# Kernel tuning notes

Measured on AMD Instinct MI355X. Metric: run time of the kernel, lower is better.

Reference implementation:

```python
import jax, jax.numpy as jnp
import numpy as np

B, CIN, H, W = 32, 64, 112, 112
COUT, KH, KW = 64, 3, 3
STRIDE = (1, 1)
PADDING = ((1, 1), (1, 1))
DILATION = (1, 1)


def setup_inputs() -> dict:
    key = jax.random.key(0)
    k1, k2, k3 = jax.random.split(key, 3)
    # quantized activations and weights, int8 value range [-128, 127]
    x_q = jax.random.randint(k1, (B, CIN, H, W), -128, 128, dtype=jnp.int32).astype(jnp.int8)
    w_q = jax.random.randint(k2, (COUT, CIN, KH, KW), -128, 128, dtype=jnp.int32).astype(jnp.int8)
    weight_scale = jnp.float32(0.02)   # per-tensor weight scale
    act_scale = jnp.float32(0.05)      # per-tensor activation scale
    bias = jax.random.normal(k3, (COUT,), dtype=jnp.float32)
    return {"x_q": x_q, "w_q": w_q, "weight_scale": weight_scale,
            "act_scale": act_scale, "bias": bias}


def reference(x_q, w_q, weight_scale, act_scale, bias):
    acc = jax.lax.conv_general_dilated(
        x_q.astype(jnp.int32), w_q.astype(jnp.int32),
        window_strides=STRIDE, padding=PADDING, rhs_dilation=DILATION,
        dimension_numbers=("NCHW", "OIHW", "NCHW"),
        preferred_element_type=jnp.int32)
    # fused dequant (per-tensor scales) + FP32 bias -> FP32 output [B, COUT, H, W]
    out = acc.astype(jnp.float32) * (act_scale * weight_scale) + bias[None, :, None, None]
    return out
```

## Files before the change

### kernel.cpp

```cpp
#include <hip/hip_runtime.h>
#include <stdint.h>

#define BATCH 32
#define CIN   64
#define HH    112
#define WW    112
#define COUT_ 64

typedef int v4i __attribute__((ext_vector_type(4)));

#define WT_OFF   0
#define ZP_OFF   36864
#define XT_OFF   65536
#define XT_NEED  (65536 + 26167296)

__global__ void wtrans_kernel(const int* __restrict__ wq, int8_t* __restrict__ wt) {
    int idx = blockIdx.x * 256 + threadIdx.x;
    int ci   = idx & 63;
    int khkw = (idx >> 6) % 9;
    int co   = idx / 576;
    wt[idx] = (int8_t)wq[co * 576 + ci * 9 + khkw];
}

__global__ void xtrans_kernel(const int* __restrict__ x, const int* __restrict__ wq,
                              int8_t* __restrict__ ws) {
    int8_t* __restrict__ xt = ws + XT_OFF;
    const int bid = blockIdx.x;
    const int tid = threadIdx.x;
    if (bid < 6272) {
        int idx  = bid * 256 + tid;
        int ci4  = idx & 15;
        int rest = idx >> 4;
        int cg   = rest % 28;
        int bh   = rest / 28;
        int h    = bh % 112;
        int b    = bh / 112;
        const v4i* gp = (const v4i*)(x + ((b * CIN + ci4 * 4) * HH + h) * WW + cg * 4);
        v4i q0 = gp[0];
        v4i q1 = gp[3136];
        v4i q2 = gp[2 * 3136];
        v4i q3 = gp[3 * 3136];
        int8_t* rowp = xt + (size_t)bh * 114 * 64;
        #pragma unroll
        for (int j = 0; j < 4; ++j) {
            uint32_t lo01 = __builtin_amdgcn_perm((uint32_t)q1[j], (uint32_t)q0[j], 0x0C0C0400u);
            uint32_t lo23 = __builtin_amdgcn_perm((uint32_t)q3[j], (uint32_t)q2[j], 0x04000C0Cu);
            int col = cg * 4 + 1 + j;
            int sd  = (((ci4 >> 2) ^ ((col >> 1) & 3)) << 2) | (ci4 & 3);
            *(uint32_t*)&rowp[col * 64 + sd * 4] = lo01 | lo23;
        }
    } else if (bid < 6720) {
        int idx  = (bid - 6272) * 256 + tid;
        int d    = idx & 15;
        int side = (idx >> 4) & 1;
        int bh   = idx >> 5;
        int col  = side ? 113 : 0;
        *(uint32_t*)&xt[((size_t)bh * 114 + col) * 64 + d * 4] = 0u;
    } else if (bid < 6728) {
        int idx = (bid - 6720) * 256 + tid;
        if (idx < 1824) *(uint32_t*)&ws[ZP_OFF + idx * 4] = 0u;
    } else {
        int idx  = (bid - 6728) * 256 + tid;
        int ci   = idx & 63;
        int khkw = (idx >> 6) % 9;
        int co   = idx / 576;
        ws[WT_OFF + idx] = (int8_t)wq[co * 576 + ci * 9 + khkw];
    }
}

__launch_bounds__(256, 4)
__global__ void conv2_kernel(const int8_t* __restrict__ ws,
                             const float*  __restrict__ wscale,
                             const float*  __restrict__ ascale,
                             const float*  __restrict__ bias,
                             float*        __restrict__ out) {
    __shared__ int8_t xs[4 * 114 * 64];

    const int tid = threadIdx.x;
    const int bt  = ((blockIdx.x & 7) * 224) + (blockIdx.x >> 3);
    const int b   = bt / 56;
    const int h0  = (bt % 56) * 2;

    const int8_t* __restrict__ xt = ws + XT_OFF;
    const int8_t* __restrict__ zp = ws + ZP_OFF;
    const int8_t* __restrict__ wt = ws + WT_OFF;

    const int lane = tid & 63;
    const int wave = tid >> 6;
    const int ln15 = lane & 15;
    const int quad = lane >> 4;

    const v4i* wrow = (const v4i*)(wt + (size_t)(wave * 16 + ln15) * 576);
    v4i a[9];
    #pragma unroll
    for (int t = 0; t < 9; ++t) a[t] = wrow[t * 4 + quad];

    #pragma unroll
    for (int i = 0; i < 8; ++i) {
        int idx = tid + i * 256;
        if (idx < 1824) {
            int row = idx / 456;
            int rem = idx - row * 456;
            int hh  = h0 - 1 + row;
            const int8_t* src = (hh >= 0 && hh < HH)
                ? xt + ((size_t)(b * HH + hh) * 7296 + rem * 16)
                : zp + rem * 16;
            __builtin_amdgcn_global_load_lds(
                (const __attribute__((address_space(1))) int*)src,
                (__attribute__((address_space(3))) int*)(&xs[idx * 16]),
                16, 0, 0);
        }
    }
    __syncthreads();

    v4i acc[2][7];
    #pragma unroll
    for (int r = 0; r < 2; ++r)
        #pragma unroll
        for (int nt = 0; nt < 7; ++nt)
            acc[r][nt] = (v4i){0, 0, 0, 0};

    #pragma unroll
    for (int rho = 0; rho < 4; ++rho) {
        #pragma unroll
        for (int kw = 0; kw < 3; ++kw) {
            const int m   = ln15 + kw;
            const int swz = (quad ^ ((m >> 1) & 3)) << 4;
            const int8_t* bp = &xs[(rho * 114 + m) * 64 + swz];
            #pragma unroll
            for (int nt = 0; nt < 7; ++nt) {
                v4i bfrag = *(const v4i*)(bp + nt * 1024);
                if (rho <= 2)
                    acc[0][nt] = __builtin_amdgcn_mfma_i32_16x16x64_i8(
                        a[rho * 3 + kw], bfrag, acc[0][nt], 0, 0, 0);
                if (rho >= 1)
                    acc[1][nt] = __builtin_amdgcn_mfma_i32_16x16x64_i8(
                        a[(rho - 1) * 3 + kw], bfrag, acc[1][nt], 0, 0, 0);
            }
        }
    }

    const float s = ascale[0] * wscale[0];
    #pragma unroll
    for (int r = 0; r < 2; ++r) {
        const int h = h0 + r;
        #pragma unroll
        for (int reg = 0; reg < 4; ++reg) {
            int co = wave * 16 + quad * 4 + reg;
            float bv = bias[co];
            float* op = out + ((size_t)(b * COUT_ + co) * HH + h) * WW;
            #pragma unroll
            for (int nt = 0; nt < 7; ++nt)
                op[nt * 16 + ln15] = (float)acc[r][nt][reg] * s + bv;
        }
    }
}

__launch_bounds__(256, 2)
__global__ void conv_kernel(const int* __restrict__ x,
                            const int8_t* __restrict__ wt,
                            const float*  __restrict__ wscale,
                            const float*  __restrict__ ascale,
                            const float*  __restrict__ bias,
                            float*        __restrict__ out) {
    __shared__ int8_t xs[4 * 114 * 72];

    const int tid = threadIdx.x;
    const int bt  = blockIdx.x;
    const int b   = bt / 56;
    const int h0  = (bt % 56) * 2;

    #pragma unroll
    for (int it = 0; it < 7; ++it) {
        int job = tid + it * 256;
        int ci4 = job & 15;
        int cg  = (job >> 4) % 28;
        int row = job / 448;
        int hh  = h0 - 1 + row;
        v4i q0 = {0,0,0,0}, q1 = {0,0,0,0}, q2 = {0,0,0,0}, q3 = {0,0,0,0};
        if (hh >= 0 && hh < HH) {
            const v4i* gp = (const v4i*)
                (x + ((size_t)(b * CIN + ci4 * 4) * HH + hh) * WW + cg * 4);
            q0 = gp[0];
            q1 = gp[3136];
            q2 = gp[2 * 3136];
            q3 = gp[3 * 3136];
        }
        #pragma unroll
        for (int j = 0; j < 4; ++j) {
            uint32_t lo01 = __builtin_amdgcn_perm((uint32_t)q1[j], (uint32_t)q0[j], 0x0C0C0400u);
            uint32_t lo23 = __builtin_amdgcn_perm((uint32_t)q3[j], (uint32_t)q2[j], 0x04000C0Cu);
            int addr = (row * 114 + cg * 4 + 1 + j) * 72 + ci4 * 4;
            *(uint32_t*)&xs[addr] = lo01 | lo23;
        }
    }
    if (tid < 128) {
        int ci4 = tid & 15;
        int col = ((tid >> 4) & 1) ? 113 : 0;
        int row = tid >> 5;
        *(uint32_t*)&xs[(row * 114 + col) * 72 + ci4 * 4] = 0u;
    }
    __syncthreads();

    const int lane = tid & 63;
    const int wave = tid >> 6;
    const int ln15 = lane & 15;
    const int quad = lane >> 4;
    const int r    = wave >> 1;
    const int coh  = wave & 1;
    const int cobase = coh * 32;

    v4i acc[2][7];
    #pragma unroll
    for (int mt = 0; mt < 2; ++mt)
        #pragma unroll
        for (int nt = 0; nt < 7; ++nt)
            acc[mt][nt] = (v4i){0, 0, 0, 0};

    const long* w64a = (const long*)(wt + (size_t)(cobase + ln15) * 576);
    const long* w64b = (const long*)(wt + (size_t)(cobase + 16 + ln15) * 576);

    #pragma unroll
    for (int kc = 0; kc < 18; ++kc) {
        const int khkw = kc >> 1;
        const int kh   = khkw / 3;
        const int kw   = khkw % 3;
        const int half = kc & 1;
        long a0 = w64a[kc * 4 + quad];
        long a1 = w64b[kc * 4 + quad];
        const int rowb  = (kh + r) * 114;
        const int cioff = half * 32 + quad * 8;
        #pragma unroll
        for (int nt = 0; nt < 7; ++nt) {
            int col = nt * 16 + ln15 + kw;
            long bfrag = *(const long*)&xs[(rowb + col) * 72 + cioff];
            acc[0][nt] = __builtin_amdgcn_mfma_i32_16x16x32_i8(a0, bfrag, acc[0][nt], 0, 0, 0);
            acc[1][nt] = __builtin_amdgcn_mfma_i32_16x16x32_i8(a1, bfrag, acc[1][nt], 0, 0, 0);
        }
    }

    const float s = ascale[0] * wscale[0];
    const int h = h0 + r;
    #pragma unroll
    for (int mt = 0; mt < 2; ++mt) {
        #pragma unroll
        for (int reg = 0; reg < 4; ++reg) {
            int co = cobase + mt * 16 + quad * 4 + reg;
            float bv = bias[co];
            float* op = out + ((size_t)(b * COUT_ + co) * HH + h) * WW;
            #pragma unroll
            for (int nt = 0; nt < 7; ++nt) {
                int wp = nt * 16 + ln15;
                op[wp] = (float)acc[mt][nt][reg] * s + bv;
            }
        }
    }
}

extern "C" void kernel_launch(void* const* d_in, const int* in_sizes, int n_in,
                              void* d_out, int out_size, void* d_ws, size_t ws_size,
                              hipStream_t stream) {
    const int*    xq     = (const int*)d_in[0];
    const int*    wq     = (const int*)d_in[1];
    const float*  wscale = (const float*)d_in[2];
    const float*  ascale = (const float*)d_in[3];
    const float*  bias   = (const float*)d_in[4];
    int8_t* ws  = (int8_t*)d_ws;
    float*  out = (float*)d_out;

    if (ws_size >= (size_t)XT_NEED) {
        xtrans_kernel<<<6872, 256, 0, stream>>>(xq, wq, ws);
        conv2_kernel<<<BATCH * 56, 256, 0, stream>>>(ws, wscale, ascale, bias, out);
    } else {
        wtrans_kernel<<<144, 256, 0, stream>>>(wq, ws);
        conv_kernel<<<BATCH * 56, 256, 0, stream>>>(xq, ws, wscale, ascale, bias, out);
    }
}
```

Baseline: 215.1 us.

## Make conv blocks process four row-pairs with double-buffered LDS prefetch

Replaces the one-tile-per-block conv kernel with one where each block handles eight output rows as four two-row tiles. The next tile's input rows are loaded into a second LDS buffer with async global-to-LDS loads while the current tile runs its MFMAs. Weight fragments and bias are also loaded once per block instead of once per tile. In exchange, LDS use doubles, occupancy drops to 2 blocks per CU, and the grid shrinks to 448 blocks, which may underfill the GPU. The full vmcnt wait at each step can also stall on the previous tile's output stores.

New measurement: 205.0 us. 4.7% less time.

```diff
diff --git a/kernel.cpp b/kernel.cpp
--- a/kernel.cpp
+++ b/kernel.cpp
@@ -13,6 +13,8 @@
 #define ZP_OFF   36864
 #define XT_OFF   65536
 #define XT_NEED  (65536 + 26167296)
+
+#define XS_TILE  29184
 
 __global__ void wtrans_kernel(const int* __restrict__ wq, int8_t* __restrict__ wt) {
     int idx = blockIdx.x * 256 + threadIdx.x;
@@ -68,18 +70,18 @@
     }
 }
 
-__launch_bounds__(256, 4)
-__global__ void conv2_kernel(const int8_t* __restrict__ ws,
+__launch_bounds__(256, 2)
+__global__ void conv3_kernel(const int8_t* __restrict__ ws,
                              const float*  __restrict__ wscale,
                              const float*  __restrict__ ascale,
                              const float*  __restrict__ bias,
                              float*        __restrict__ out) {
-    __shared__ int8_t xs[4 * 114 * 64];
+    __shared__ int8_t xs[2][XS_TILE];
 
     const int tid = threadIdx.x;
-    const int bt  = ((blockIdx.x & 7) * 224) + (blockIdx.x >> 3);
-    const int b   = bt / 56;
-    const int h0  = (bt % 56) * 2;
+    const int bt     = ((blockIdx.x & 7) * 56) + (blockIdx.x >> 3);
+    const int b      = bt / 14;
+    const int h0base = (bt % 14) * 8;
 
     const int8_t* __restrict__ xt = ws + XT_OFF;
     const int8_t* __restrict__ zp = ws + ZP_OFF;
@@ -95,64 +97,90 @@
     #pragma unroll
     for (int t = 0; t < 9; ++t) a[t] = wrow[t * 4 + quad];
 
-    #pragma unroll
-    for (int i = 0; i < 8; ++i) {
-        int idx = tid + i * 256;
-        if (idx < 1824) {
-            int row = idx / 456;
-            int rem = idx - row * 456;
-            int hh  = h0 - 1 + row;
-            const int8_t* src = (hh >= 0 && hh < HH)
-                ? xt + ((size_t)(b * HH + hh) * 7296 + rem * 16)
-                : zp + rem * 16;
-            __builtin_amdgcn_global_load_lds(
-                (const __attribute__((address_space(1))) int*)src,
-                (__attribute__((address_space(3))) int*)(&xs[idx * 16]),
-                16, 0, 0);
-        }
-    }
-    __syncthreads();
-
-    v4i acc[2][7];
-    #pragma unroll
-    for (int r = 0; r < 2; ++r)
-        #pragma unroll
-        for (int nt = 0; nt < 7; ++nt)
-            acc[r][nt] = (v4i){0, 0, 0, 0};
-
-    #pragma unroll
-    for (int rho = 0; rho < 4; ++rho) {
-        #pragma unroll
-        for (int kw = 0; kw < 3; ++kw) {
-            const int m   = ln15 + kw;
-            const int swz = (quad ^ ((m >> 1) & 3)) << 4;
-            const int8_t* bp = &xs[(rho * 114 + m) * 64 + swz];
-            #pragma unroll
-            for (int nt = 0; nt < 7; ++nt) {
-                v4i bfrag = *(const v4i*)(bp + nt * 1024);
-                if (rho <= 2)
-                    acc[0][nt] = __builtin_amdgcn_mfma_i32_16x16x64_i8(
-                        a[rho * 3 + kw], bfrag, acc[0][nt], 0, 0, 0);
-                if (rho >= 1)
-                    acc[1][nt] = __builtin_amdgcn_mfma_i32_16x16x64_i8(
-                        a[(rho - 1) * 3 + kw], bfrag, acc[1][nt], 0, 0, 0);
+    const float s = ascale[0] * wscale[0];
+    float bv[4];
+    #pragma unroll
+    for (int reg = 0; reg < 4; ++reg) bv[reg] = bias[wave * 16 + quad * 4 + reg];
+
+    auto stage = [&](int buf, int t) {
+        const int h0 = h0base + 2 * t;
+        #pragma unroll
+        for (int i = 0; i < 8; ++i) {
+            int idx = tid + i * 256;
+            if (idx < 1824) {
+                int row = idx / 456;
+                int rem = idx - row * 456;
+                int hh  = h0 - 1 + row;
+                const int8_t* src = (hh >= 0 && hh < HH)
+                    ? xt + ((size_t)(b * HH + hh) * 7296 + rem * 16)
+                    : zp + rem * 16;
+                __builtin_amdgcn_global_load_lds(
+                    (const __attribute__((address_space(1))) int*)src,
+                    (__attribute__((address_space(3))) int*)(&xs[buf][idx * 16]),
+                    16, 0, 0);
             }
         }
-    }
-
-    const float s = ascale[0] * wscale[0];
-    #pragma unroll
-    for (int r = 0; r < 2; ++r) {
-        const int h = h0 + r;
-        #pragma unroll
-        for (int reg = 0; reg < 4; ++reg) {
-            int co = wave * 16 + quad * 4 + reg;
-            float bv = bias[co];
-            float* op = out + ((size_t)(b * COUT_ + co) * HH + h) * WW;
+    };
+
+    stage(0, 0);
+    asm volatile("s_waitcnt vmcnt(0)" ::: "memory");
+    __builtin_amdgcn_s_barrier();
+    __builtin_amdgcn_sched_barrier(0);
+
+    int cur = 0;
+    #pragma unroll 1
+    for (int t = 0; t < 4; ++t) {
+        if (t < 3) stage(cur ^ 1, t + 1);
+
+        v4i acc[2][7];
+        #pragma unroll
+        for (int r = 0; r < 2; ++r)
             #pragma unroll
             for (int nt = 0; nt < 7; ++nt)
-                op[nt * 16 + ln15] = (float)acc[r][nt][reg] * s + bv;
-        }
+                acc[r][nt] = (v4i){0, 0, 0, 0};
+
+        const int8_t* xsb = &xs[cur][0];
+        #pragma unroll
+        for (int rho = 0; rho < 4; ++rho) {
+            #pragma unroll
+            for (int kw = 0; kw < 3; ++kw) {
+                const int m   = ln15 + kw;
+                const int swz = (quad ^ ((m >> 1) & 3)) << 4;
+                const int8_t* bp = &xsb[(rho * 114 + m) * 64 + swz];
+                #pragma unroll
+                for (int nt = 0; nt < 7; ++nt) {
+                    v4i bfrag = *(const v4i*)(bp + nt * 1024);
+                    if (rho <= 2)
+                        acc[0][nt] = __builtin_amdgcn_mfma_i32_16x16x64_i8(
+                            a[rho * 3 + kw], bfrag, acc[0][nt], 0, 0, 0);
+                    if (rho >= 1)
+                        acc[1][nt] = __builtin_amdgcn_mfma_i32_16x16x64_i8(
+                            a[(rho - 1) * 3 + kw], bfrag, acc[1][nt], 0, 0, 0);
+                }
+            }
+        }
+
+        __builtin_amdgcn_sched_barrier(0);
+        if (t < 3) {
+            asm volatile("s_waitcnt vmcnt(0)" ::: "memory");
+            __builtin_amdgcn_s_barrier();
+            __builtin_amdgcn_sched_barrier(0);
+        }
+
+        const int h0 = h0base + 2 * t;
+        #pragma unroll
+        for (int r = 0; r < 2; ++r) {
+            const int h = h0 + r;
+            #pragma unroll
+            for (int reg = 0; reg < 4; ++reg) {
+                int co = wave * 16 + quad * 4 + reg;
+                float* op = out + ((size_t)(b * COUT_ + co) * HH + h) * WW;
+                #pragma unroll
+                for (int nt = 0; nt < 7; ++nt)
+                    op[nt * 16 + ln15] = (float)acc[r][nt][reg] * s + bv[reg];
+            }
+        }
+        cur ^= 1;
     }
 }
 
@@ -270,7 +298,7 @@
 
     if (ws_size >= (size_t)XT_NEED) {
         xtrans_kernel<<<6872, 256, 0, stream>>>(xq, wq, ws);
-        conv2_kernel<<<BATCH * 56, 256, 0, stream>>>(ws, wscale, ascale, bias, out);
+        conv3_kernel<<<448, 256, 0, stream>>>(ws, wscale, ascale, bias, out);
     } else {
         wtrans_kernel<<<144, 256, 0, stream>>>(wq, ws);
         conv_kernel<<<BATCH * 56, 256, 0, stream>>>(xq, ws, wscale, ascale, bias, out);
```
